# Kernel tuning notes

Measured on AMD Instinct MI355X. Metric: run time of the kernel, lower is better.

The kernel has to match this reference:

```python
import jax, jax.numpy as jnp
import numpy as np
import math

B, T, C, F = 8, 2048, 1024, 4096
N_LAYER, LAYER_ID = 12, 1


def _init_params(key):
    ks = jax.random.split(key, 16)
    s = 0.02
    ratio_0_to_1 = LAYER_ID / (N_LAYER - 1)
    ratio_1_to_almost0 = 1.0 - LAYER_ID / N_LAYER
    h = np.arange(C, dtype=np.float32)
    decay = -5.0 + 8.0 * (h / (C - 1)) ** (0.7 + 1.3 * ratio_0_to_1)
    zigzag = np.array([((i + 1) % 3 - 1) for i in range(C)], dtype=np.float32) * 0.5
    first = np.ones(C, dtype=np.float32) * math.log(0.3) + zigzag
    xi = (np.arange(C, dtype=np.float32) / C)
    p = {
        'ln1_w': jnp.ones(C), 'ln1_b': jnp.zeros(C),
        'ln2_w': jnp.ones(C), 'ln2_b': jnp.zeros(C),
        'att_time_decay': jnp.asarray(decay),
        'att_time_first': jnp.asarray(first),
        'att_mix_k': jnp.asarray(xi ** ratio_1_to_almost0),
        'att_mix_v': jnp.asarray(xi ** ratio_1_to_almost0 + 0.3 * ratio_0_to_1),
        'att_mix_r': jnp.asarray(xi ** (0.5 * ratio_1_to_almost0)),
        'att_Wk': jax.random.normal(ks[0], (C, C)) * s,
        'att_Wv': jax.random.normal(ks[1], (C, C)) * s,
        'att_Wr': jax.random.normal(ks[2], (C, C)) * s,
        'att_Wo': jax.random.normal(ks[3], (C, C)) * s,
        'ffn_mix_k': jnp.asarray(xi ** ratio_1_to_almost0),
        'ffn_mix_r': jnp.asarray(xi ** ratio_1_to_almost0),
        'ffn_Wk': jax.random.normal(ks[4], (F, C)) * s,
        'ffn_Wr': jax.random.normal(ks[5], (C, C)) * s,
        'ffn_Wv': jax.random.normal(ks[6], (C, F)) * s,
        'short_W': jax.random.normal(ks[7], (C, C)) * s,
    }
    return p


def setup_inputs() -> dict:
    key = jax.random.key(0)
    k1, k2 = jax.random.split(key)
    inp = {'x': jax.random.normal(k1, (B, T, C), dtype=jnp.float32)}
    inp.update(_init_params(k2))
    return inp


def _layernorm(x, w, b, eps=1e-5):
    mu = jnp.mean(x, axis=-1, keepdims=True)
    var = jnp.var(x, axis=-1, keepdims=True)
    return (x - mu) * jax.lax.rsqrt(var + eps) * w + b


def _time_shift(x):
    # ZeroPad2d((0,0,1,-1)): prepend zero row along T, drop last
    return jnp.pad(x, ((0, 0), (1, 0), (0, 0)))[:, :-1]


def _wkv(time_decay, time_first, k, v):
    # numerically-stable WKV recurrence, matching the CUDA kernel math
    w = -jnp.exp(time_decay)  # [C]
    u = time_first            # [C]
    kt = jnp.swapaxes(k, 0, 1)  # [T,B,C]
    vt = jnp.swapaxes(v, 0, 1)
    a0 = jnp.zeros(k.shape[::2] if False else (k.shape[0], k.shape[2]), k.dtype)
    b0 = jnp.zeros_like(a0)
    p0 = jnp.full_like(a0, -1e30)

    def step(carry, kv):
        a, b, p = carry
        k_t, v_t = kv
        ww = u + k_t
        q = jnp.maximum(p, ww)
        e1 = jnp.exp(p - q)
        e2 = jnp.exp(ww - q)
        y = (e1 * a + e2 * v_t) / (e1 * b + e2)
        ww2 = p + w
        q2 = jnp.maximum(ww2, k_t)
        f1 = jnp.exp(ww2 - q2)
        f2 = jnp.exp(k_t - q2)
        return (f1 * a + f2 * v_t, f1 * b + f2, q2), y

    _, ys = jax.lax.scan(step, (a0, b0, p0), (kt, vt))
    return jnp.swapaxes(ys, 0, 1)  # [B,T,C]


def _lin(x, W):
    return jnp.einsum('btc,oc->bto', x, W)


def reference(x, ln1_w, ln1_b, ln2_w, ln2_b,
              att_time_decay, att_time_first, att_mix_k, att_mix_v, att_mix_r,
              att_Wk, att_Wv, att_Wr, att_Wo,
              ffn_mix_k, ffn_mix_r, ffn_Wk, ffn_Wr, ffn_Wv, short_W):
    # --- TimeMix on ln1(x) ---
    h = _layernorm(x, ln1_w, ln1_b)
    hh = _time_shift(h)
    xk = h * att_mix_k + hh * (1 - att_mix_k)
    xv = h * att_mix_v + hh * (1 - att_mix_v)
    xr = h * att_mix_r + hh * (1 - att_mix_r)
    k = _lin(xk, att_Wk)
    v = _lin(xv, att_Wv)
    sr = jax.nn.sigmoid(_lin(xr, att_Wr))
    rwkv = sr * _wkv(att_time_decay, att_time_first, k, v)
    att_out = _lin(rwkv, att_Wo)
    # shortcut linear replaces identity residual (L3TC Block)
    x = _lin(x, short_W) + att_out
    # --- ChannelMix on ln2(x) ---
    g = _layernorm(x, ln2_w, ln2_b)
    gg = _time_shift(g)
    gk = g * ffn_mix_k + gg * (1 - ffn_mix_k)
    gr = g * ffn_mix_r + gg * (1 - ffn_mix_r)
    kk = jnp.square(jax.nn.relu(_lin(gk, ffn_Wk)))
    kv = _lin(kk, ffn_Wv)
    rkv = jax.nn.sigmoid(_lin(gr, ffn_Wr)) * kv
    return x + rkv
```

## Files before the change

kernel.cpp:

```cpp
#include <hip/hip_runtime.h>

#define BB 8
#define TT 2048
#define CC 1024
#define FF 4096
#define MM (BB*TT)

typedef unsigned short u16;
typedef __bf16 bf16x8 __attribute__((ext_vector_type(8)));
typedef float f32x4 __attribute__((ext_vector_type(4)));

__device__ __forceinline__ u16 f2bf(float f) {
  unsigned int u = __float_as_uint(f);
  u += 0x7fffu + ((u >> 16) & 1u);
  return (u16)(u >> 16);
}
__device__ __forceinline__ float bf2f(u16 h) {
  unsigned int u = ((unsigned int)h) << 16;
  return __uint_as_float(u);
}
__device__ __forceinline__ float sigm(float x) { return 1.f / (1.f + __expf(-x)); }

__device__ __forceinline__ void async16(const void* g, void* l) {
  __builtin_amdgcn_global_load_lds(
      (const __attribute__((address_space(1))) unsigned int*)g,
      (__attribute__((address_space(3))) unsigned int*)l, 16, 0, 0);
}

#define GROUP_M 16

#define DSRD(d, a, o) \
  asm volatile("ds_read_b128 %0, %1 offset:%c2" : "=v"(d) : "v"(a), "i"(o))

#define MFMA16(A_, B_, C_) \
  (C_) = __builtin_amdgcn_mfma_f32_16x16x32_bf16( \
      __builtin_bit_cast(bf16x8, (A_)), __builtin_bit_cast(bf16x8, (B_)), (C_), 0, 0, 0)

#define SCHED0  __builtin_amdgcn_sched_barrier(0)
#define BARRIER __builtin_amdgcn_s_barrier()
#define LGKM(n) asm volatile("s_waitcnt lgkmcnt(" #n ")")

#define READ_A4(bank, BETA, MH, KH) do { \
  DSRD(bank[0], aAddr##KH, (BETA)*32768 + ((MH)*4+0)*2048); \
  DSRD(bank[1], aAddr##KH, (BETA)*32768 + ((MH)*4+1)*2048); \
  DSRD(bank[2], aAddr##KH, (BETA)*32768 + ((MH)*4+2)*2048); \
  DSRD(bank[3], aAddr##KH, (BETA)*32768 + ((MH)*4+3)*2048); \
} while (0)

#define READ_B2(bank, BETA, NP, KH) do { \
  DSRD(bank[0], bAddr##KH, (BETA)*32768 + (NP)*16384 + 0*2048); \
  DSRD(bank[1], bAddr##KH, (BETA)*32768 + (NP)*16384 + 1*2048); \
} while (0)

#define MFMA8(ABANK, BBANK, AO, NO) do { \
  _Pragma("unroll") \
  for (int mi = 0; mi < 4; ++mi) \
    _Pragma("unroll") \
    for (int ni = 0; ni < 2; ++ni) \
      MFMA16(ABANK[mi], BBANK[ni], acc[(AO)+mi][(NO)+ni]); \
} while (0)

#define EXEC8(ABANK, BBANK, AO, NO) do { \
  SCHED0; __builtin_amdgcn_s_setprio(1); \
  MFMA8(ABANK, BBANK, AO, NO); \
  __builtin_amdgcn_s_setprio(0); SCHED0; } while (0)

#define TILE(BETA, T2A, DOSTAGE, RDNEXT, GATE4) do { \
   \
  READ_B2(bQ, BETA, 1, 0); \
  LGKM(2); EXEC8(aX, bP, 0, 0); BARRIER; SCHED0; \
   \
  READ_A4(aZ, BETA, 0, 1); \
  LGKM(6); EXEC8(aY, bP, 4, 0); BARRIER; SCHED0; \
   \
  READ_B2(bP, BETA, 0, 1); \
  LGKM(6); EXEC8(aY, bQ, 4, 2); BARRIER; SCHED0; \
   \
  LGKM(6); EXEC8(aX, bQ, 0, 2); BARRIER; SCHED0; \
   \
  READ_A4(aY, BETA, 1, 1); \
  LGKM(4); SCHED0; \
  if (DOSTAGE) { stA(BETA, 0, T2A); stB(BETA, 0, T2A); } \
  EXEC8(aZ, bP, 0, 0); BARRIER; SCHED0; \
   \
  READ_B2(bQ, BETA, 1, 1); \
  LGKM(2); SCHED0; \
  if (DOSTAGE) { stA(BETA, 1, T2A); stB(BETA, 1, T2A); } \
  EXEC8(aY, bP, 4, 0); \
  if (GATE4) asm volatile("s_waitcnt vmcnt(4)"); \
  else       asm volatile("s_waitcnt vmcnt(0)"); \
  BARRIER; SCHED0; \
   \
  if (RDNEXT) { READ_A4(aX, (BETA)^1, 0, 0); READ_B2(bP, (BETA)^1, 0, 0); LGKM(6); } \
  else LGKM(0); \
  SCHED0; \
  if (DOSTAGE) { stA(BETA, 2, T2A); stB(BETA, 2, T2A); } \
  EXEC8(aY, bQ, 4, 2); BARRIER; SCHED0; \
   \
  if (RDNEXT) { READ_A4(aY, (BETA)^1, 1, 0); LGKM(10); } \
  else LGKM(0); \
  SCHED0; \
  if (DOSTAGE) { stA(BETA, 3, T2A); stB(BETA, 3, T2A); } \
  EXEC8(aZ, bQ, 0, 2); BARRIER; SCHED0; \
} while (0)

template<int MODE>
__global__ __launch_bounds__(512, 2) void gemm_bt(
    const u16* __restrict__ A, const u16* __restrict__ W,
    float* __restrict__ Cf, u16* __restrict__ Cb,
    const u16* __restrict__ R, int N, int K)
{
  __shared__ __align__(16) u16 ldsA[2][256 * 64];
  __shared__ __align__(16) u16 ldsB[2][256 * 64];

  const int tid  = threadIdx.x;
  const int wave = tid >> 6;
  const int lane = tid & 63;
  const int wmi  = wave >> 2;
  const int wni  = wave & 3;
  const int lm   = lane & 15;
  const int lq   = lane >> 4;

  const int bid  = blockIdx.x + blockIdx.y * gridDim.x;
  const int gsz  = GROUP_M * gridDim.y;
  const int gid  = bid / gsz;
  const int rem  = bid - gid * gsz;
  const int bm   = (gid * GROUP_M + (rem % GROUP_M)) * 256;
  const int bn   = (rem / GROUP_M) * 256;

  const int NT = K >> 6;

  const int ls     = lane >> 3;
  const int schunk = (lane & 7) ^ ls;
  const int rowA   = wave * 8 + ls;
  const int rowB   = (wave >> 2) * 64 + (wave & 3) * 8 + ls;
  const u16* gA = A + (size_t)(bm + rowA) * K + schunk * 8;
  const u16* gB = W + (size_t)(bn + rowB) * K + schunk * 8;
  const size_t rowK = (size_t)64 * K;

  auto stA = [&](int buf, int q, int t2) {
    async16(gA + (size_t)t2 * 64 + (size_t)q * rowK,
            &ldsA[buf][(q * 64 + wave * 8) * 64]);
  };
  auto stB = [&](int buf, int q, int t2) {
    const int qrow = (q == 0) ? 0 : (q == 1) ? 128 : (q == 2) ? 32 : 160;
    async16(gB + (size_t)t2 * 64 + (size_t)qrow * K,
            &ldsB[buf][(q * 64 + wave * 8) * 64]);
  };

  const unsigned lAbase =
      (unsigned)(size_t)(const __attribute__((address_space(3))) u16*)&ldsA[0][0];
  const unsigned lBbase =
      (unsigned)(size_t)(const __attribute__((address_space(3))) u16*)&ldsB[0][0];
  const unsigned aAddr0 = lAbase + (unsigned)((wmi * 128 + lm) * 128 + (((lq    ) ^ (lm & 7)) * 16));
  const unsigned aAddr1 = lAbase + (unsigned)((wmi * 128 + lm) * 128 + (((lq + 4) ^ (lm & 7)) * 16));
  const unsigned bAddr0 = lBbase + (unsigned)((wni * 32 + lm) * 128 + (((lq    ) ^ (lm & 7)) * 16));
  const unsigned bAddr1 = lBbase + (unsigned)((wni * 32 + lm) * 128 + (((lq + 4) ^ (lm & 7)) * 16));

  f32x4 acc[8][4] = {};
  f32x4 aX[4], aY[4], aZ[4], bP[2], bQ[2];

  stA(0, 0, 0); stA(0, 1, 0); stA(0, 2, 0); stA(0, 3, 0);
  stB(0, 0, 0); stB(0, 1, 0); stB(0, 2, 0); stB(0, 3, 0);
  stA(1, 0, 1); stA(1, 1, 1); stA(1, 2, 1); stA(1, 3, 1);
  stB(1, 0, 1); stB(1, 1, 1); stB(1, 2, 1); stB(1, 3, 1);
  asm volatile("s_waitcnt vmcnt(0)");
  BARRIER;
  READ_A4(aX, 0, 0, 0);
  READ_A4(aY, 0, 1, 0);
  READ_B2(bP, 0, 0, 0);
  SCHED0;

  for (int t = 0; t + 3 < NT; t += 2) {
    TILE(0, t + 2, 1, 1, 1);
    TILE(1, t + 3, 1, 1, 1);
  }

  TILE(0, 0, 0, 1, 0);
  TILE(1, 0, 0, 0, 0);

  const int row0 = bm + wmi * 128 + lq * 4;
  const int col0 = bn + wni * 64 + lm;
#pragma unroll
  for (int mi = 0; mi < 8; ++mi)
#pragma unroll
    for (int ni = 0; ni < 4; ++ni) {
      size_t base = (size_t)(row0 + mi * 16) * N + (col0 + ni * 16);
#pragma unroll
      for (int r2 = 0; r2 < 4; ++r2) {
        size_t idx = base + (size_t)r2 * N;
        float v = acc[mi][ni][r2];
        if (MODE == 0) Cf[idx] = v;
        if (MODE == 2) { float rl = v > 0.f ? v : 0.f; Cb[idx] = f2bf(rl * rl); }
        if (MODE == 3) Cb[idx] = f2bf(v);
        if (MODE == 4) Cf[idx] += sigm(bf2f(R[idx])) * v;
      }
    }
}

__global__ __launch_bounds__(256) void prep_mix(
    const float* __restrict__ x,
    const float* __restrict__ lnw, const float* __restrict__ lnb,
    const float* __restrict__ mk, const float* __restrict__ mv, const float* __restrict__ mr,
    u16* __restrict__ ok, u16* __restrict__ ov, u16* __restrict__ orr,
    u16* __restrict__ oxb)
{
  const int m = blockIdx.x;
  const int t = m & (TT - 1);
  const int tid = threadIdx.x;
  const int wave = tid >> 6, lane = tid & 63;
  const bool hasp = (t != 0);

  const float4 xc4 = ((const float4*)(x + (size_t)m * CC))[tid];
  float4 xp4 = make_float4(0.f, 0.f, 0.f, 0.f);
  if (hasp) xp4 = ((const float4*)(x + (size_t)(m - 1) * CC))[tid];

  float s0 = xc4.x + xc4.y + xc4.z + xc4.w;
  float s1 = xc4.x*xc4.x + xc4.y*xc4.y + xc4.z*xc4.z + xc4.w*xc4.w;
  float s2 = xp4.x + xp4.y + xp4.z + xp4.w;
  float s3 = xp4.x*xp4.x + xp4.y*xp4.y + xp4.z*xp4.z + xp4.w*xp4.w;
#pragma unroll
  for (int off2 = 32; off2 > 0; off2 >>= 1) {
    s0 += __shfl_xor(s0, off2);
    s1 += __shfl_xor(s1, off2);
    s2 += __shfl_xor(s2, off2);
    s3 += __shfl_xor(s3, off2);
  }
  __shared__ float red[4][4];
  if (lane == 0) { red[0][wave] = s0; red[1][wave] = s1; red[2][wave] = s2; red[3][wave] = s3; }
  __syncthreads();
  const float S0 = red[0][0] + red[0][1] + red[0][2] + red[0][3];
  const float S1 = red[1][0] + red[1][1] + red[1][2] + red[1][3];
  const float S2 = red[2][0] + red[2][1] + red[2][2] + red[2][3];
  const float S3 = red[3][0] + red[3][1] + red[3][2] + red[3][3];
  const float inv = 1.f / (float)CC;
  const float muc = S0 * inv, varc = S1 * inv - muc * muc, rsc = rsqrtf(varc + 1e-5f);
  const float mup = S2 * inv, varp = S3 * inv - mup * mup, rsp = rsqrtf(varp + 1e-5f);

  const float xc[4] = {xc4.x, xc4.y, xc4.z, xc4.w};
  const float xp[4] = {xp4.x, xp4.y, xp4.z, xp4.w};
  const float4 lw4 = ((const float4*)lnw)[tid];
  const float4 lb4 = ((const float4*)lnb)[tid];
  const float lw[4] = {lw4.x, lw4.y, lw4.z, lw4.w};
  const float lb[4] = {lb4.x, lb4.y, lb4.z, lb4.w};
  const float4 mk4 = ((const float4*)mk)[tid];
  const float mka[4] = {mk4.x, mk4.y, mk4.z, mk4.w};
  const float4 mr4 = ((const float4*)mr)[tid];
  const float mra[4] = {mr4.x, mr4.y, mr4.z, mr4.w};
  float mva[4] = {0.f, 0.f, 0.f, 0.f};
  if (ov) {
    const float4 mv4 = ((const float4*)mv)[tid];
    mva[0] = mv4.x; mva[1] = mv4.y; mva[2] = mv4.z; mva[3] = mv4.w;
  }

  ushort4 wk2, wv2, wr2, wb2;
  u16* pk = (u16*)&wk2; u16* pv = (u16*)&wv2; u16* pr = (u16*)&wr2; u16* pb = (u16*)&wb2;
#pragma unroll
  for (int j = 0; j < 4; ++j) {
    float h  = (xc[j] - muc) * rsc * lw[j] + lb[j];
    float hh = hasp ? (xp[j] - mup) * rsp * lw[j] + lb[j] : 0.f;
    pk[j] = f2bf(h * mka[j] + hh * (1.f - mka[j]));
    pv[j] = f2bf(h * mva[j] + hh * (1.f - mva[j]));
    pr[j] = f2bf(h * mra[j] + hh * (1.f - mra[j]));
    pb[j] = f2bf(xc[j]);
  }
  ((ushort4*)(ok + (size_t)m * CC))[tid] = wk2;
  if (ov)  ((ushort4*)(ov  + (size_t)m * CC))[tid] = wv2;
  ((ushort4*)(orr + (size_t)m * CC))[tid] = wr2;
  if (oxb) ((ushort4*)(oxb + (size_t)m * (2 * CC)))[tid] = wb2;
}

#define WKV_CPB 32
#define WKV_NCH 32
#define WKV_L   (TT / WKV_NCH)

__global__ __launch_bounds__(1024) void wkv_scan(
    const u16* __restrict__ k, const u16* __restrict__ v, const u16* __restrict__ r,
    const float* __restrict__ decay, const float* __restrict__ first,
    u16* __restrict__ out)
{
  const int b  = blockIdx.x >> 5;
  const int c0 = (blockIdx.x & 31) * WKV_CPB;
  const int tid = threadIdx.x;
  const int cl = tid & 31;
  const int j  = tid >> 5;
  const int c  = c0 + cl;

  const float w   = -__expf(decay[c]);
  const float lam = __expf(w);
  const float eu  = __expf(first[c]);

  const size_t base  = (size_t)b * TT * CC + (size_t)j * WKV_L * CC + c;
  size_t obase = ((size_t)b * TT + (size_t)j * WKV_L) * (2 * CC) + c;

  float a = 0.f, bb = 0.f;
  size_t idx = base;
  for (int i = 0; i < WKV_L; ++i, idx += CC) {
    const float kt = bf2f(k[idx]), vt = bf2f(v[idx]);
    const float ek = __expf(kt);
    a  = fmaf(lam, a, ek * vt);
    bb = fmaf(lam, bb, ek);
  }

  __shared__ float sA[WKV_NCH][WKV_CPB];
  __shared__ float sB[WKV_NCH][WKV_CPB];
  sA[j][cl] = a; sB[j][cl] = bb;
  __syncthreads();
  if (tid < WKV_CPB) {
    float ca = 0.f, cb = 0.f;
    const float cw   = -__expf(decay[c0 + tid]);
    const float cLam = __expf(cw * (float)WKV_L);
#pragma unroll
    for (int q = 0; q < WKV_NCH; ++q) {
      const float ta = sA[q][tid], tb = sB[q][tid];
      sA[q][tid] = ca; sB[q][tid] = cb;
      ca = fmaf(cLam, ca, ta);
      cb = fmaf(cLam, cb, tb);
    }
  }
  __syncthreads();
  a = sA[j][cl]; bb = sB[j][cl];

  idx = base;
  for (int i = 0; i < WKV_L; ++i, idx += CC, obase += 2 * CC) {
    const float kt = bf2f(k[idx]), vt = bf2f(v[idx]), rt = bf2f(r[idx]);
    const float ek = __expf(kt);
    const float e2 = eu * ek;
    const float y  = (a + e2 * vt) / (bb + e2);
    out[obase] = f2bf(sigm(rt) * y);
    a  = fmaf(lam, a, ek * vt);
    bb = fmaf(lam, bb, ek);
  }
}

struct ConvArgs { const float* src[8]; int end[8]; int dstoff[8]; };

__global__ __launch_bounds__(256) void conv_w(ConvArgs args, u16* __restrict__ dst)
{
  const int i = (blockIdx.x * 256 + threadIdx.x) * 4;
  int seg = 0;
  const float* sp = args.src[0];
  int base = 0;
#pragma unroll
  for (int s = 1; s < 8; ++s) {
    if (i >= args.end[s - 1]) { seg = s; sp = args.src[s]; base = args.end[s - 1]; }
  }
  const int l = i - base;
  const float4 vv = *(const float4*)(sp + l);
  int dsti;
  if (seg == 3)      { int row = l >> 10, col = l & 1023; dsti = args.dstoff[3] + row * 2048 + 1024 + col; }
  else if (seg == 4) { int row = l >> 10, col = l & 1023; dsti = args.dstoff[4] + row * 2048 + col; }
  else               dsti = args.dstoff[seg] + l;
  ushort4 d;
  d.x = f2bf(vv.x); d.y = f2bf(vv.y); d.z = f2bf(vv.z); d.w = f2bf(vv.w);
  *(ushort4*)(dst + dsti) = d;
}

extern "C" void kernel_launch(void* const* d_in, const int* in_sizes, int n_in,
                              void* d_out, int out_size, void* d_ws, size_t ws_size,
                              hipStream_t stream)
{
  const float* x    = (const float*)d_in[0];
  const float* ln1w = (const float*)d_in[1];
  const float* ln1b = (const float*)d_in[2];
  const float* ln2w = (const float*)d_in[3];
  const float* ln2b = (const float*)d_in[4];
  const float* tdec = (const float*)d_in[5];
  const float* tfir = (const float*)d_in[6];
  const float* amk  = (const float*)d_in[7];
  const float* amv  = (const float*)d_in[8];
  const float* amr  = (const float*)d_in[9];
  const float* Wk   = (const float*)d_in[10];
  const float* Wv   = (const float*)d_in[11];
  const float* Wr   = (const float*)d_in[12];
  const float* Wo   = (const float*)d_in[13];
  const float* fmk  = (const float*)d_in[14];
  const float* fmr  = (const float*)d_in[15];
  const float* WfK  = (const float*)d_in[16];
  const float* WfR  = (const float*)d_in[17];
  const float* WfV  = (const float*)d_in[18];
  const float* Wsh  = (const float*)d_in[19];
  float* out = (float*)d_out;
  char* ws = (char*)d_ws;

  u16* wW = (u16*)(ws);
  u16* U0 = (u16*)(ws + 29360128);
  u16* U1 = (u16*)(ws + 62914560);
  u16* U2 = (u16*)(ws + 96468992);
  u16* U3 = (u16*)(ws + 130023424);
  u16* U4 = (u16*)(ws + 163577856);

  u16* xk   = U0;
  u16* xv   = U1;
  u16* xr   = U2;
  u16* Ap   = U4;
  u16* kbuf = U3;
  u16* vbuf = U0;
  u16* rbuf = U1;
  u16* gk   = U0;
  u16* gr   = U1;
  u16* kkb  = U2;
  u16* rffn = U0;

  u16* bWk   = wW + 0;
  u16* bWv   = wW + 1048576;
  u16* bWr   = wW + 2097152;
  u16* bWsWo = wW + 3145728;
  u16* bWfR  = wW + 5242880;
  u16* bWfK  = wW + 6291456;
  u16* bWfV  = wW + 10485760;

  ConvArgs ca;
  ca.src[0] = Wk;  ca.src[1] = Wv;  ca.src[2] = Wr;  ca.src[3] = Wo;
  ca.src[4] = Wsh; ca.src[5] = WfR; ca.src[6] = WfK; ca.src[7] = WfV;
  const int e = 1048576;
  ca.end[0] = e;     ca.end[1] = 2*e;  ca.end[2] = 3*e;  ca.end[3] = 4*e;
  ca.end[4] = 5*e;   ca.end[5] = 6*e;  ca.end[6] = 10*e; ca.end[7] = 14*e;
  ca.dstoff[0] = 0;     ca.dstoff[1] = e;    ca.dstoff[2] = 2*e;
  ca.dstoff[3] = 3*e;   ca.dstoff[4] = 3*e;
  ca.dstoff[5] = 5*e;   ca.dstoff[6] = 6*e;  ca.dstoff[7] = 10*e;

  conv_w<<<14336, 256, 0, stream>>>(ca, wW);
  prep_mix<<<MM, 256, 0, stream>>>(x, ln1w, ln1b, amk, amv, amr, xk, xv, xr, Ap);

  dim3 g8(MM / 256, CC / 256);
  gemm_bt<3><<<g8, 512, 0, stream>>>(xk, bWk, nullptr, kbuf, nullptr, CC, CC);
  gemm_bt<3><<<g8, 512, 0, stream>>>(xv, bWv, nullptr, vbuf, nullptr, CC, CC);
  gemm_bt<3><<<g8, 512, 0, stream>>>(xr, bWr, nullptr, rbuf, nullptr, CC, CC);

  wkv_scan<<<BB * (CC / WKV_CPB), 1024, 0, stream>>>(kbuf, vbuf, rbuf, tdec, tfir, Ap + CC);

  gemm_bt<0><<<g8, 512, 0, stream>>>(Ap, bWsWo, out, nullptr, nullptr, CC, 2 * CC);

  prep_mix<<<MM, 256, 0, stream>>>(out, ln2w, ln2b, fmk, nullptr, fmr, gk, nullptr, gr, nullptr);

  dim3 gF(MM / 256, FF / 256);
  gemm_bt<2><<<gF, 512, 0, stream>>>(gk, bWfK, nullptr, kkb, nullptr, FF, CC);
  gemm_bt<3><<<g8, 512, 0, stream>>>(gr, bWfR, nullptr, rffn, nullptr, CC, CC);
  gemm_bt<4><<<g8, 512, 0, stream>>>(kkb, bWfV, out, nullptr, rffn, CC, FF);
}
```

Baseline: 925.8 us.

## Reschedule GEMM tile pipeline with two A banks and four B banks, fewer barriers

Restructures the per-K-tile schedule of the bf16 MFMA GEMM. Operand registers change from three A banks and two B banks to two A banks and four B banks. LDS reads and async global-to-LDS staging are interleaved differently, and each tile now uses two workgroup barriers instead of eight. The aim is less barrier stall time and better overlap of LDS reads and global loads with MFMA work. In exchange the lgkmcnt/vmcnt wait counts must stay exactly right, and the new register footprint could change occupancy.

```diff
diff --git a/kernel.cpp b/kernel.cpp
--- a/kernel.cpp
+++ b/kernel.cpp
@@ -61,47 +61,38 @@
 } while (0)
 
 #define EXEC8(ABANK, BBANK, AO, NO) do { \
-  SCHED0; __builtin_amdgcn_s_setprio(1); \
+  __builtin_amdgcn_s_setprio(1); \
   MFMA8(ABANK, BBANK, AO, NO); \
   __builtin_amdgcn_s_setprio(0); SCHED0; } while (0)
 
-#define TILE(BETA, T2A, DOSTAGE, RDNEXT, GATE4) do { \
-   \
-  READ_B2(bQ, BETA, 1, 0); \
-  LGKM(2); EXEC8(aX, bP, 0, 0); BARRIER; SCHED0; \
-   \
-  READ_A4(aZ, BETA, 0, 1); \
-  LGKM(6); EXEC8(aY, bP, 4, 0); BARRIER; SCHED0; \
-   \
-  READ_B2(bP, BETA, 0, 1); \
-  LGKM(6); EXEC8(aY, bQ, 4, 2); BARRIER; SCHED0; \
-   \
-  LGKM(6); EXEC8(aX, bQ, 0, 2); BARRIER; SCHED0; \
-   \
-  READ_A4(aY, BETA, 1, 1); \
-  LGKM(4); SCHED0; \
-  if (DOSTAGE) { stA(BETA, 0, T2A); stB(BETA, 0, T2A); } \
-  EXEC8(aZ, bP, 0, 0); BARRIER; SCHED0; \
-   \
-  READ_B2(bQ, BETA, 1, 1); \
-  LGKM(2); SCHED0; \
-  if (DOSTAGE) { stA(BETA, 1, T2A); stB(BETA, 1, T2A); } \
-  EXEC8(aY, bP, 4, 0); \
-  if (GATE4) asm volatile("s_waitcnt vmcnt(4)"); \
-  else       asm volatile("s_waitcnt vmcnt(0)"); \
+#define TILE(BETA, T2A, ST, RD) do { \
+   READ_A4(aB, BETA, 1, 0); \
+  LGKM(6); SCHED0; EXEC8(aA, bP, 0, 0); \
+   READ_B2(bR, BETA, 0, 1); \
+  LGKM(6); SCHED0; EXEC8(aA, bQ, 0, 2); \
+   READ_A4(aA, BETA, 0, 1); \
+  LGKM(6); SCHED0; EXEC8(aB, bQ, 4, 2); \
   BARRIER; SCHED0; \
    \
-  if (RDNEXT) { READ_A4(aX, (BETA)^1, 0, 0); READ_B2(bP, (BETA)^1, 0, 0); LGKM(6); } \
-  else LGKM(0); \
-  SCHED0; \
-  if (DOSTAGE) { stA(BETA, 2, T2A); stB(BETA, 2, T2A); } \
-  EXEC8(aY, bQ, 4, 2); BARRIER; SCHED0; \
+  READ_B2(bS, BETA, 1, 1); \
+  if (ST) { stB(BETA, 0, T2A); stB(BETA, 1, T2A); \
+            stA(BETA, 0, T2A); stA(BETA, 2, T2A); } \
+  LGKM(6); SCHED0; EXEC8(aB, bP, 4, 0); \
+   READ_A4(aB, BETA, 1, 1); \
+  LGKM(6); SCHED0; EXEC8(aA, bR, 0, 0); \
+  if (ST) asm volatile("s_waitcnt vmcnt(4)"); \
+  else    asm volatile("s_waitcnt vmcnt(0)"); \
+  BARRIER; SCHED0; \
    \
-  if (RDNEXT) { READ_A4(aY, (BETA)^1, 1, 0); LGKM(10); } \
-  else LGKM(0); \
-  SCHED0; \
-  if (DOSTAGE) { stA(BETA, 3, T2A); stB(BETA, 3, T2A); } \
-  EXEC8(aZ, bQ, 0, 2); BARRIER; SCHED0; \
+  if (RD) READ_B2(bP, (BETA)^1, 0, 0); \
+  if (ST) { stB(BETA, 2, T2A); stB(BETA, 3, T2A); \
+            stA(BETA, 1, T2A); stA(BETA, 3, T2A); } \
+  if (RD) LGKM(6); else LGKM(4); \
+  SCHED0; EXEC8(aA, bS, 0, 2); \
+   if (RD) { READ_A4(aA, (BETA)^1, 0, 0); LGKM(6); } else LGKM(0); \
+  SCHED0; EXEC8(aB, bS, 4, 2); \
+   if (RD) { READ_B2(bQ, (BETA)^1, 1, 0); LGKM(8); } else LGKM(0); \
+  SCHED0; EXEC8(aB, bR, 4, 0); \
 } while (0)
 
 template<int MODE>
@@ -158,7 +149,7 @@
   const unsigned bAddr1 = lBbase + (unsigned)((wni * 32 + lm) * 128 + (((lq + 4) ^ (lm & 7)) * 16));
 
   f32x4 acc[8][4] = {};
-  f32x4 aX[4], aY[4], aZ[4], bP[2], bQ[2];
+  f32x4 aA[4], aB[4], bP[2], bQ[2], bR[2], bS[2];
 
   stA(0, 0, 0); stA(0, 1, 0); stA(0, 2, 0); stA(0, 3, 0);
   stB(0, 0, 0); stB(0, 1, 0); stB(0, 2, 0); stB(0, 3, 0);
@@ -166,18 +157,18 @@
   stB(1, 0, 1); stB(1, 1, 1); stB(1, 2, 1); stB(1, 3, 1);
   asm volatile("s_waitcnt vmcnt(0)");
   BARRIER;
-  READ_A4(aX, 0, 0, 0);
-  READ_A4(aY, 0, 1, 0);
+  READ_A4(aA, 0, 0, 0);
   READ_B2(bP, 0, 0, 0);
-  SCHED0;
+  READ_B2(bQ, 0, 1, 0);
+  LGKM(0); SCHED0;
 
   for (int t = 0; t + 3 < NT; t += 2) {
-    TILE(0, t + 2, 1, 1, 1);
-    TILE(1, t + 3, 1, 1, 1);
-  }
-
-  TILE(0, 0, 0, 1, 0);
-  TILE(1, 0, 0, 0, 0);
+    TILE(0, t + 2, 1, 1);
+    TILE(1, t + 3, 1, 1);
+  }
+
+  TILE(0, 0, 0, 1);
+  TILE(1, 0, 0, 0);
 
   const int row0 = bm + wmi * 128 + lq * 4;
   const int col0 = bn + wni * 64 + lm;
```

Result: faster. 796.4 us (-14.0%).
